# Optimization experiments

Measured on AMD Instinct MI355X. Metric: run time of the kernel, lower is better.

The kernel has to match this reference:

```python
import jax, jax.numpy as jnp
import numpy as np

IN_DIMS = 32
HID = 64
N_HIDDEN = 5  # tcnn n_hidden_layers = hidden_layers + 1 = 5
OUT_DIMS = 3
BATCH = 2097152


def setup_inputs() -> dict:
    key = jax.random.key(0)
    ks = jax.random.split(key, N_HIDDEN + 2)
    x = jax.random.normal(ks[0], (BATCH, IN_DIMS), dtype=jnp.float32)
    # tcnn FullyFusedMLP has no biases; Kaiming-ish init scale
    W0 = jax.random.normal(ks[1], (IN_DIMS, HID), dtype=jnp.float32) * (1.0 / np.sqrt(IN_DIMS))
    Wh = jax.random.normal(ks[2], (N_HIDDEN - 1, HID, HID), dtype=jnp.float32) * (1.0 / np.sqrt(HID))
    Wo = jax.random.normal(ks[3], (HID, OUT_DIMS), dtype=jnp.float32) * (1.0 / np.sqrt(HID))
    return {"x": x, "W0": W0, "Wh": Wh, "Wo": Wo}


def reference(x, W0, Wh, Wo):
    # input layer -> ReLU
    h = jax.nn.relu(x @ W0)  # [B, 64]
    # 4 more hidden layers of 64->64 with ReLU (small fixed count, unrolled)
    for i in range(Wh.shape[0]):
        h = jax.nn.relu(h @ Wh[i])
    # linear output layer (output_activation = None)
    return h @ Wo  # [B, 3]
```

## Files before the change

kernel.cpp:

```cpp
#include <hip/hip_runtime.h>


typedef __attribute__((ext_vector_type(8))) short short8;
typedef __attribute__((ext_vector_type(4))) float f32x4;

#define BATCH       2097152
#define NTILES      (BATCH / 16)
#define NBLOCKS     512
#define TOTAL_WAVES (NBLOCKS * 4)
#define ITERS       (NTILES / TOTAL_WAVES)

static_assert(NTILES % TOTAL_WAVES == 0, "tile count must divide evenly");

__device__ __forceinline__ short f2bf_rne(float f) {
    unsigned u = __builtin_bit_cast(unsigned, f);
    u += 0x7FFFu + ((u >> 16) & 1u);
    return (short)(u >> 16);
}

__device__ __forceinline__ unsigned pack2(float a, float b) {
    unsigned ua = __builtin_bit_cast(unsigned, a) + 0x8000u;
    unsigned ub = __builtin_bit_cast(unsigned, b) + 0x8000u;
    return __builtin_amdgcn_perm(ub, ua, 0x07060302u);
}

__global__ __launch_bounds__(256, 2)
void mlp_fused(const float* __restrict__ x, const float* __restrict__ W0,
               const float* __restrict__ Wh, const float* __restrict__ Wo,
               float* __restrict__ out)
{
    __shared__ __align__(16) unsigned char smem[4 * 2048];

    const int tid  = threadIdx.x;
    const int wave = tid >> 6;
    const int lane = tid & 63;
    const int n = lane & 15;
    const int q = lane >> 4;

    short8 wf[38];
    #pragma unroll
    for (int t = 0; t < 4; ++t) {
        const float* p = W0 + (8 * q) * 64 + 16 * t + n;
        short8 f;
        #pragma unroll
        for (int j = 0; j < 8; ++j) f[j] = f2bf_rne(p[j * 64]);
        wf[t] = f;
    }
    #pragma unroll
    for (int l = 0; l < 4; ++l) {
        #pragma unroll
        for (int t = 0; t < 4; ++t) {
            #pragma unroll
            for (int c = 0; c < 2; ++c) {
                const float* p = Wh + l * 4096 + (32 * c + 8 * q) * 64 + 16 * t + n;
                short8 f;
                #pragma unroll
                for (int j = 0; j < 8; ++j) f[j] = f2bf_rne(p[j * 64]);
                wf[4 + l * 8 + t * 2 + c] = f;
            }
        }
    }
    #pragma unroll
    for (int c = 0; c < 2; ++c) {
        short8 f;
        #pragma unroll
        for (int j = 0; j < 8; ++j)
            f[j] = (n < 3) ? f2bf_rne(Wo[(32 * c + 8 * q + j) * 3 + n]) : (short)0;
        wf[36 + c] = f;
    }

    const unsigned lbase = (unsigned)wave * 2048u + (unsigned)n * 128u;
    unsigned waddr[4], raddr[2];
    #pragma unroll
    for (int t = 0; t < 4; ++t)
        waddr[t] = lbase + 32u * (unsigned)(t ^ (n & 3)) + 8u * (unsigned)q;
    #pragma unroll
    for (int c = 0; c < 2; ++c)
        raddr[c] = lbase + 32u * (unsigned)((2 * c + (q >> 1)) ^ (n & 3)) + 16u * (unsigned)(q & 1);

    const unsigned gw = blockIdx.x * 4 + wave;
    const f32x4* xp = (const f32x4*)(x + (size_t)(gw * 16 + n) * 32 + 8 * q);
    const size_t xstep = (size_t)TOTAL_WAVES * 16 * 32 / 4;

    f32x4 pa = xp[0], pb = xp[1];
    const f32x4 z = {0.f, 0.f, 0.f, 0.f};

    for (int it = 0; it < ITERS; ++it) {
        f32x4 ca = pa, cb = pb;
        if (it + 1 < ITERS) {
            pa = xp[(size_t)(it + 1) * xstep];
            pb = xp[(size_t)(it + 1) * xstep + 1];
        }

        union { unsigned u[4]; short8 s; } bin;
        bin.u[0] = pack2(ca[0], ca[1]);
        bin.u[1] = pack2(ca[2], ca[3]);
        bin.u[2] = pack2(cb[0], cb[1]);
        bin.u[3] = pack2(cb[2], cb[3]);

        f32x4 acc[4];
        #pragma unroll
        for (int t = 0; t < 4; ++t)
            acc[t] = __builtin_amdgcn_mfma_f32_16x16x32_bf16(wf[t], bin.s, z, 0, 0, 0);

        #pragma unroll
        for (int s = 0; s < 5; ++s) {
            #pragma unroll
            for (int t = 0; t < 4; ++t) {
                float a0 = fmaxf(acc[t][0], 0.f);
                float a1 = fmaxf(acc[t][1], 0.f);
                float a2 = fmaxf(acc[t][2], 0.f);
                float a3 = fmaxf(acc[t][3], 0.f);
                uint2 wv;
                wv.x = pack2(a0, a1);
                wv.y = pack2(a2, a3);
                *(uint2*)(smem + waddr[t]) = wv;
            }
            short8 b0 = *(const short8*)(smem + raddr[0]);
            short8 b1 = *(const short8*)(smem + raddr[1]);

            if (s < 4) {
                #pragma unroll
                for (int t = 0; t < 4; ++t) {
                    acc[t] = __builtin_amdgcn_mfma_f32_16x16x32_bf16(
                                 wf[4 + s * 8 + t * 2 + 0], b0, z, 0, 0, 0);
                    acc[t] = __builtin_amdgcn_mfma_f32_16x16x32_bf16(
                                 wf[4 + s * 8 + t * 2 + 1], b1, acc[t], 0, 0, 0);
                }
            } else {
                f32x4 o = __builtin_amdgcn_mfma_f32_16x16x32_bf16(wf[36], b0, z, 0, 0, 0);
                o = __builtin_amdgcn_mfma_f32_16x16x32_bf16(wf[37], b1, o, 0, 0, 0);
                if (lane < 16) {
                    size_t row = ((size_t)gw + (size_t)it * TOTAL_WAVES) * 16 + lane;
                    float* po = out + row * 3;
                    po[0] = o[0];
                    po[1] = o[1];
                    po[2] = o[2];
                }
            }
        }
    }
}

extern "C" void kernel_launch(void* const* d_in, const int* in_sizes, int n_in,
                              void* d_out, int out_size, void* d_ws, size_t ws_size,
                              hipStream_t stream) {
    (void)in_sizes; (void)n_in; (void)d_ws; (void)ws_size; (void)out_size;
    const float* x  = (const float*)d_in[0];
    const float* W0 = (const float*)d_in[1];
    const float* Wh = (const float*)d_in[2];
    const float* Wo = (const float*)d_in[3];
    float* out = (float*)d_out;
    mlp_fused<<<NBLOCKS, 256, 0, stream>>>(x, W0, Wh, Wo, out);
}
```

Baseline: 463.3 us.

## Process two 16-row tiles per wave iteration to interleave MFMA chains

Each wave now handles two independent 16-row tiles per loop iteration, interleaving their MFMA chains and LDS round-trips so one tile's dependency latency is hidden by the other's work. The grid is doubled to 1024 blocks, each block takes twice the LDS, and the prefetch loads both tiles' inputs. The cost is higher register pressure from the doubled accumulators and prefetch buffers on top of the 38 resident weight fragments, which could cut occupancy or cause spills under launch_bounds(256,2).

```diff
diff --git a/kernel.cpp b/kernel.cpp
--- a/kernel.cpp
+++ b/kernel.cpp
@@ -6,11 +6,12 @@
 
 #define BATCH       2097152
 #define NTILES      (BATCH / 16)
-#define NBLOCKS     512
+#define NBLOCKS     1024
 #define TOTAL_WAVES (NBLOCKS * 4)
-#define ITERS       (NTILES / TOTAL_WAVES)
+#define TPI         2
+#define ITERS       (NTILES / (TOTAL_WAVES * TPI))
 
-static_assert(NTILES % TOTAL_WAVES == 0, "tile count must divide evenly");
+static_assert(NTILES % (TOTAL_WAVES * TPI) == 0, "tile count must divide evenly");
 
 __device__ __forceinline__ short f2bf_rne(float f) {
     unsigned u = __builtin_bit_cast(unsigned, f);
@@ -29,7 +30,7 @@
                const float* __restrict__ Wh, const float* __restrict__ Wo,
                float* __restrict__ out)
 {
-    __shared__ __align__(16) unsigned char smem[4 * 2048];
+    __shared__ __align__(16) unsigned char smem[4 * TPI * 2048];
 
     const int tid  = threadIdx.x;
     const int wave = tid >> 6;
@@ -69,7 +70,7 @@
         wf[36 + c] = f;
     }
 
-    const unsigned lbase = (unsigned)wave * 2048u + (unsigned)n * 128u;
+    const unsigned lbase = (unsigned)wave * (TPI * 2048u) + (unsigned)n * 128u;
     unsigned waddr[4], raddr[2];
     #pragma unroll
     for (int t = 0; t < 4; ++t)
@@ -79,64 +80,88 @@
         raddr[c] = lbase + 32u * (unsigned)((2 * c + (q >> 1)) ^ (n & 3)) + 16u * (unsigned)(q & 1);
 
     const unsigned gw = blockIdx.x * 4 + wave;
-    const f32x4* xp = (const f32x4*)(x + (size_t)(gw * 16 + n) * 32 + 8 * q);
-    const size_t xstep = (size_t)TOTAL_WAVES * 16 * 32 / 4;
+    const f32x4* xp = (const f32x4*)(x + (size_t)(gw * 2 * 16 + n) * 32 + 8 * q);
+    const size_t xstep = (size_t)TOTAL_WAVES * TPI * 16 * 32 / 4;
+    const size_t xtile = 16 * 32 / 4;
 
-    f32x4 pa = xp[0], pb = xp[1];
+    f32x4 pf[TPI][2];
+    pf[0][0] = xp[0];         pf[0][1] = xp[1];
+    pf[1][0] = xp[xtile];     pf[1][1] = xp[xtile + 1];
     const f32x4 z = {0.f, 0.f, 0.f, 0.f};
 
     for (int it = 0; it < ITERS; ++it) {
-        f32x4 ca = pa, cb = pb;
+        f32x4 cur[TPI][2];
+        #pragma unroll
+        for (int u = 0; u < TPI; ++u) { cur[u][0] = pf[u][0]; cur[u][1] = pf[u][1]; }
         if (it + 1 < ITERS) {
-            pa = xp[(size_t)(it + 1) * xstep];
-            pb = xp[(size_t)(it + 1) * xstep + 1];
+            const f32x4* np = xp + (size_t)(it + 1) * xstep;
+            pf[0][0] = np[0];        pf[0][1] = np[1];
+            pf[1][0] = np[xtile];    pf[1][1] = np[xtile + 1];
         }
 
-        union { unsigned u[4]; short8 s; } bin;
-        bin.u[0] = pack2(ca[0], ca[1]);
-        bin.u[1] = pack2(ca[2], ca[3]);
-        bin.u[2] = pack2(cb[0], cb[1]);
-        bin.u[3] = pack2(cb[2], cb[3]);
+        f32x4 acc[TPI][4];
+        #pragma unroll
+        for (int u = 0; u < TPI; ++u) {
+            union { unsigned w[4]; short8 s; } bin;
+            bin.w[0] = pack2(cur[u][0][0], cur[u][0][1]);
+            bin.w[1] = pack2(cur[u][0][2], cur[u][0][3]);
+            bin.w[2] = pack2(cur[u][1][0], cur[u][1][1]);
+            bin.w[3] = pack2(cur[u][1][2], cur[u][1][3]);
+            #pragma unroll
+            for (int t = 0; t < 4; ++t)
+                acc[u][t] = __builtin_amdgcn_mfma_f32_16x16x32_bf16(wf[t], bin.s, z, 0, 0, 0);
+        }
 
-        f32x4 acc[4];
-        #pragma unroll
-        for (int t = 0; t < 4; ++t)
-            acc[t] = __builtin_amdgcn_mfma_f32_16x16x32_bf16(wf[t], bin.s, z, 0, 0, 0);
-
+        short8 b[TPI][2];
         #pragma unroll
         for (int s = 0; s < 5; ++s) {
             #pragma unroll
-            for (int t = 0; t < 4; ++t) {
-                float a0 = fmaxf(acc[t][0], 0.f);
-                float a1 = fmaxf(acc[t][1], 0.f);
-                float a2 = fmaxf(acc[t][2], 0.f);
-                float a3 = fmaxf(acc[t][3], 0.f);
-                uint2 wv;
-                wv.x = pack2(a0, a1);
-                wv.y = pack2(a2, a3);
-                *(uint2*)(smem + waddr[t]) = wv;
+            for (int u = 0; u < TPI; ++u) {
+                #pragma unroll
+                for (int t = 0; t < 4; ++t) {
+                    float a0 = fmaxf(acc[u][t][0], 0.f);
+                    float a1 = fmaxf(acc[u][t][1], 0.f);
+                    float a2 = fmaxf(acc[u][t][2], 0.f);
+                    float a3 = fmaxf(acc[u][t][3], 0.f);
+                    uint2 wv;
+                    wv.x = pack2(a0, a1);
+                    wv.y = pack2(a2, a3);
+                    *(uint2*)(smem + waddr[t] + u * 2048) = wv;
+                }
             }
-            short8 b0 = *(const short8*)(smem + raddr[0]);
-            short8 b1 = *(const short8*)(smem + raddr[1]);
-
+            #pragma unroll
+            for (int u = 0; u < TPI; ++u) {
+                b[u][0] = *(const short8*)(smem + raddr[0] + u * 2048);
+                b[u][1] = *(const short8*)(smem + raddr[1] + u * 2048);
+            }
             if (s < 4) {
                 #pragma unroll
-                for (int t = 0; t < 4; ++t) {
-                    acc[t] = __builtin_amdgcn_mfma_f32_16x16x32_bf16(
-                                 wf[4 + s * 8 + t * 2 + 0], b0, z, 0, 0, 0);
-                    acc[t] = __builtin_amdgcn_mfma_f32_16x16x32_bf16(
-                                 wf[4 + s * 8 + t * 2 + 1], b1, acc[t], 0, 0, 0);
+                for (int u = 0; u < TPI; ++u) {
+                    #pragma unroll
+                    for (int t = 0; t < 4; ++t) {
+                        acc[u][t] = __builtin_amdgcn_mfma_f32_16x16x32_bf16(
+                                        wf[4 + s * 8 + t * 2 + 0], b[u][0], z, 0, 0, 0);
+                        acc[u][t] = __builtin_amdgcn_mfma_f32_16x16x32_bf16(
+                                        wf[4 + s * 8 + t * 2 + 1], b[u][1], acc[u][t], 0, 0, 0);
+                    }
                 }
-            } else {
-                f32x4 o = __builtin_amdgcn_mfma_f32_16x16x32_bf16(wf[36], b0, z, 0, 0, 0);
-                o = __builtin_amdgcn_mfma_f32_16x16x32_bf16(wf[37], b1, o, 0, 0, 0);
-                if (lane < 16) {
-                    size_t row = ((size_t)gw + (size_t)it * TOTAL_WAVES) * 16 + lane;
-                    float* po = out + row * 3;
-                    po[0] = o[0];
-                    po[1] = o[1];
-                    po[2] = o[2];
-                }
+            }
+        }
+
+        f32x4 o[TPI];
+        #pragma unroll
+        for (int u = 0; u < TPI; ++u) {
+            o[u] = __builtin_amdgcn_mfma_f32_16x16x32_bf16(wf[36], b[u][0], z, 0, 0, 0);
+            o[u] = __builtin_amdgcn_mfma_f32_16x16x32_bf16(wf[37], b[u][1], o[u], 0, 0, 0);
+        }
+        if (lane < 16) {
+            size_t t0 = ((size_t)it * TOTAL_WAVES + gw) * 2;
+            #pragma unroll
+            for (int u = 0; u < TPI; ++u) {
+                float* po = out + ((t0 + u) * 16 + lane) * 3;
+                po[0] = o[u][0];
+                po[1] = o[u][1];
+                po[2] = o[u][2];
             }
         }
     }
```

New measurement: 455.5 us. Within noise of the previous version (-1.7%).

## Split hidden-neuron tiles across waves with shared double-buffered activations

Applied to the files above, without the earlier changes.

Each wave now holds weights for only one 16-neuron output slice of every layer instead of all 64, which cuts per-thread weight registers roughly fourfold. This lets occupancy rise from 2 to 4 blocks per CU and the grid grow to 2048 blocks. Blocks process 64 rows cooperatively, exchanging activations through a double-buffered, swizzled LDS tile. The cost is a block-wide barrier after every layer instead of purely wave-local work. The x prefetch for the next iteration is also moved later in the layer chain.

```diff
diff --git a/kernel.cpp b/kernel.cpp
--- a/kernel.cpp
+++ b/kernel.cpp
@@ -4,13 +4,11 @@
 typedef __attribute__((ext_vector_type(8))) short short8;
 typedef __attribute__((ext_vector_type(4))) float f32x4;
 
-#define BATCH       2097152
-#define NTILES      (BATCH / 16)
-#define NBLOCKS     512
-#define TOTAL_WAVES (NBLOCKS * 4)
-#define ITERS       (NTILES / TOTAL_WAVES)
-
-static_assert(NTILES % TOTAL_WAVES == 0, "tile count must divide evenly");
+#define BATCH   2097152
+#define NBLOCKS 2048
+#define ROWS    64
+#define ITERS   (BATCH / (NBLOCKS * ROWS))
+static_assert(BATCH % (NBLOCKS * ROWS) == 0, "");
 
 __device__ __forceinline__ short f2bf_rne(float f) {
     unsigned u = __builtin_bit_cast(unsigned, f);
@@ -24,40 +22,36 @@
     return __builtin_amdgcn_perm(ub, ua, 0x07060302u);
 }
 
-__global__ __launch_bounds__(256, 2)
+__global__ __launch_bounds__(256, 4)
 void mlp_fused(const float* __restrict__ x, const float* __restrict__ W0,
                const float* __restrict__ Wh, const float* __restrict__ Wo,
                float* __restrict__ out)
 {
-    __shared__ __align__(16) unsigned char smem[4 * 2048];
+    __shared__ __align__(16) unsigned char smem[2][ROWS * 128];
 
     const int tid  = threadIdx.x;
-    const int wave = tid >> 6;
+    const int w    = tid >> 6;
     const int lane = tid & 63;
     const int n = lane & 15;
     const int q = lane >> 4;
 
-    short8 wf[38];
-    #pragma unroll
-    for (int t = 0; t < 4; ++t) {
-        const float* p = W0 + (8 * q) * 64 + 16 * t + n;
+    short8 wf0, wfh[4][2], wfo[2];
+    {
+        const float* p = W0 + (8 * q) * 64 + 16 * w + n;
         short8 f;
         #pragma unroll
         for (int j = 0; j < 8; ++j) f[j] = f2bf_rne(p[j * 64]);
-        wf[t] = f;
+        wf0 = f;
     }
     #pragma unroll
     for (int l = 0; l < 4; ++l) {
         #pragma unroll
-        for (int t = 0; t < 4; ++t) {
+        for (int c = 0; c < 2; ++c) {
+            const float* p = Wh + l * 4096 + (32 * c + 8 * q) * 64 + 16 * w + n;
+            short8 f;
             #pragma unroll
-            for (int c = 0; c < 2; ++c) {
-                const float* p = Wh + l * 4096 + (32 * c + 8 * q) * 64 + 16 * t + n;
-                short8 f;
-                #pragma unroll
-                for (int j = 0; j < 8; ++j) f[j] = f2bf_rne(p[j * 64]);
-                wf[4 + l * 8 + t * 2 + c] = f;
-            }
+            for (int j = 0; j < 8; ++j) f[j] = f2bf_rne(p[j * 64]);
+            wfh[l][c] = f;
         }
     }
     #pragma unroll
@@ -66,79 +60,91 @@
         #pragma unroll
         for (int j = 0; j < 8; ++j)
             f[j] = (n < 3) ? f2bf_rne(Wo[(32 * c + 8 * q + j) * 3 + n]) : (short)0;
-        wf[36 + c] = f;
+        wfo[c] = f;
     }
 
-    const unsigned lbase = (unsigned)wave * 2048u + (unsigned)n * 128u;
-    unsigned waddr[4], raddr[2];
-    #pragma unroll
-    for (int t = 0; t < 4; ++t)
-        waddr[t] = lbase + 32u * (unsigned)(t ^ (n & 3)) + 8u * (unsigned)q;
-    #pragma unroll
-    for (int c = 0; c < 2; ++c)
-        raddr[c] = lbase + 32u * (unsigned)((2 * c + (q >> 1)) ^ (n & 3)) + 16u * (unsigned)(q & 1);
+    const int m7 = n & 7;
+    const unsigned wbase = (unsigned)n * 128u
+                         + 16u * (unsigned)((2 * w + (q >> 1)) ^ m7)
+                         + 8u * (unsigned)(q & 1);
+    const unsigned r0 = (unsigned)n * 128u + 16u * (unsigned)((q) ^ m7);
+    const unsigned r1 = (unsigned)n * 128u + 16u * (unsigned)((4 + q) ^ m7);
 
-    const unsigned gw = blockIdx.x * 4 + wave;
-    const f32x4* xp = (const f32x4*)(x + (size_t)(gw * 16 + n) * 32 + 8 * q);
-    const size_t xstep = (size_t)TOTAL_WAVES * 16 * 32 / 4;
+    const f32x4 z = {0.f, 0.f, 0.f, 0.f};
+    f32x4 xa[4][2];
 
-    f32x4 pa = xp[0], pb = xp[1];
-    const f32x4 z = {0.f, 0.f, 0.f, 0.f};
+    auto load_x = [&](int it) {
+        const size_t base = ((size_t)it * NBLOCKS + blockIdx.x) * ROWS;
+        #pragma unroll
+        for (int j = 0; j < 4; ++j) {
+            const f32x4* xp = (const f32x4*)(x + (base + 16 * j + n) * 32) + 2 * q;
+            xa[j][0] = xp[0];
+            xa[j][1] = xp[1];
+        }
+    };
+
+    load_x(0);
 
     for (int it = 0; it < ITERS; ++it) {
-        f32x4 ca = pa, cb = pb;
-        if (it + 1 < ITERS) {
-            pa = xp[(size_t)(it + 1) * xstep];
-            pb = xp[(size_t)(it + 1) * xstep + 1];
-        }
-
-        union { unsigned u[4]; short8 s; } bin;
-        bin.u[0] = pack2(ca[0], ca[1]);
-        bin.u[1] = pack2(ca[2], ca[3]);
-        bin.u[2] = pack2(cb[0], cb[1]);
-        bin.u[3] = pack2(cb[2], cb[3]);
+        const size_t base = ((size_t)it * NBLOCKS + blockIdx.x) * ROWS;
 
         f32x4 acc[4];
         #pragma unroll
-        for (int t = 0; t < 4; ++t)
-            acc[t] = __builtin_amdgcn_mfma_f32_16x16x32_bf16(wf[t], bin.s, z, 0, 0, 0);
+        for (int j = 0; j < 4; ++j) {
+            union { unsigned u[4]; short8 s; } bin;
+            bin.u[0] = pack2(xa[j][0][0], xa[j][0][1]);
+            bin.u[1] = pack2(xa[j][0][2], xa[j][0][3]);
+            bin.u[2] = pack2(xa[j][1][0], xa[j][1][1]);
+            bin.u[3] = pack2(xa[j][1][2], xa[j][1][3]);
+            acc[j] = __builtin_amdgcn_mfma_f32_16x16x32_bf16(wf0, bin.s, z, 0, 0, 0);
+        }
 
         #pragma unroll
         for (int s = 0; s < 5; ++s) {
+            unsigned char* buf = smem[s & 1];
+
             #pragma unroll
-            for (int t = 0; t < 4; ++t) {
-                float a0 = fmaxf(acc[t][0], 0.f);
-                float a1 = fmaxf(acc[t][1], 0.f);
-                float a2 = fmaxf(acc[t][2], 0.f);
-                float a3 = fmaxf(acc[t][3], 0.f);
+            for (int j = 0; j < 4; ++j) {
                 uint2 wv;
-                wv.x = pack2(a0, a1);
-                wv.y = pack2(a2, a3);
-                *(uint2*)(smem + waddr[t]) = wv;
+                wv.x = pack2(fmaxf(acc[j][0], 0.f), fmaxf(acc[j][1], 0.f));
+                wv.y = pack2(fmaxf(acc[j][2], 0.f), fmaxf(acc[j][3], 0.f));
+                *(uint2*)(buf + wbase + j * 2048) = wv;
             }
-            short8 b0 = *(const short8*)(smem + raddr[0]);
-            short8 b1 = *(const short8*)(smem + raddr[1]);
+
+            if (s == 4 && it + 1 < ITERS) load_x(it + 1);
+
+            __syncthreads();
 
             if (s < 4) {
+                short8 b0[4], b1[4];
                 #pragma unroll
-                for (int t = 0; t < 4; ++t) {
-                    acc[t] = __builtin_amdgcn_mfma_f32_16x16x32_bf16(
-                                 wf[4 + s * 8 + t * 2 + 0], b0, z, 0, 0, 0);
-                    acc[t] = __builtin_amdgcn_mfma_f32_16x16x32_bf16(
-                                 wf[4 + s * 8 + t * 2 + 1], b1, acc[t], 0, 0, 0);
-                }
+                for (int j = 0; j < 4; ++j)
+                    b0[j] = *(const short8*)(buf + r0 + j * 2048);
+                #pragma unroll
+                for (int j = 0; j < 4; ++j)
+                    b1[j] = *(const short8*)(buf + r1 + j * 2048);
+                #pragma unroll
+                for (int j = 0; j < 4; ++j)
+                    acc[j] = __builtin_amdgcn_mfma_f32_16x16x32_bf16(
+                                 wfh[s][0], b0[j], z, 0, 0, 0);
+                #pragma unroll
+                for (int j = 0; j < 4; ++j)
+                    acc[j] = __builtin_amdgcn_mfma_f32_16x16x32_bf16(
+                                 wfh[s][1], b1[j], acc[j], 0, 0, 0);
             } else {
-                f32x4 o = __builtin_amdgcn_mfma_f32_16x16x32_bf16(wf[36], b0, z, 0, 0, 0);
-                o = __builtin_amdgcn_mfma_f32_16x16x32_bf16(wf[37], b1, o, 0, 0, 0);
+                short8 c0 = *(const short8*)(buf + r0 + w * 2048);
+                short8 c1 = *(const short8*)(buf + r1 + w * 2048);
+                f32x4 o = __builtin_amdgcn_mfma_f32_16x16x32_bf16(wfo[0], c0, z, 0, 0, 0);
+                o = __builtin_amdgcn_mfma_f32_16x16x32_bf16(wfo[1], c1, o, 0, 0, 0);
                 if (lane < 16) {
-                    size_t row = ((size_t)gw + (size_t)it * TOTAL_WAVES) * 16 + lane;
-                    float* po = out + row * 3;
+                    float* po = out + (base + 16 * w + lane) * 3;
                     po[0] = o[0];
                     po[1] = o[1];
                     po[2] = o[2];
                 }
             }
         }
+        __syncthreads();
     }
 }
 
```

Measured after the change: 442.7 us. 4.5% less time.
